# Kernel tuning notes

Hardware: AMD Instinct MI355X
Metric: run time of the kernel (lower is better)

Reference implementation:

```python
import jax, jax.numpy as jnp
import numpy as np


def _rgcn_layer(h, Wr, Ws, src, dst, rel, norm):
    # h: [N,d], Wr: [R,d,d] per-relation weight, Ws: [d,d] self-loop weight
    N, d = h.shape
    R = Wr.shape[0]
    E = src.shape[0]
    msg = jnp.zeros((E, d), h.dtype)
    for r in range(R):  # R is small/static; transform-then-gather per relation
        hW = h @ Wr[r]              # [N,d]
        msg = jnp.where((rel == r)[:, None], hW[src], msg)  # [E,d]
    agg = jax.ops.segment_sum(msg * norm[:, None], dst, num_segments=N)
    return jax.nn.relu(agg + h @ Ws)


def _calc_score(emb, w_relation, es, er, eo):
    # DistMult-style bilinear score: s^T W_r o per target edge
    s = emb[es]                     # [T,d]
    o = emb[eo]                     # [T,d]
    R = w_relation.shape[0]
    sW = jnp.zeros_like(s)
    for r in range(R):
        sW = jnp.where((er == r)[:, None], s @ w_relation[r], sW)
    return jnp.sum(sW * o, axis=-1)  # [T]


def setup_inputs() -> dict:
    key = jax.random.key(0)
    ks = jax.random.split(key, 16)
    N, E, T, d, R, L = 20000, 160000, 50000, 768, 8, 2
    sc = 1.0 / np.sqrt(d)
    return {
        "node_feat": jax.random.normal(ks[0], (N, d), jnp.float32),
        "edge_norm": jax.random.uniform(ks[1], (E,), jnp.float32),
        "W_rel": jax.random.normal(ks[2], (L, R, d, d), jnp.float32) * sc,
        "W_self": jax.random.normal(ks[3], (L, d, d), jnp.float32) * sc,
        "w_relation": jax.random.normal(ks[4], (R, d, d), jnp.float32) * sc,
        "src": jax.random.randint(ks[5], (E,), 0, N, jnp.int32),
        "dst": jax.random.randint(ks[6], (E,), 0, N, jnp.int32),
        "rel": jax.random.randint(ks[7], (E,), 0, R, jnp.int32),
        "pos_src": jax.random.randint(ks[8], (T,), 0, N, jnp.int32),
        "pos_rel": jax.random.randint(ks[9], (T,), 0, R, jnp.int32),
        "pos_dst": jax.random.randint(ks[10], (T,), 0, N, jnp.int32),
        "neg_src": jax.random.randint(ks[11], (T,), 0, N, jnp.int32),
        "neg_rel": jax.random.randint(ks[12], (T,), 0, R, jnp.int32),
        "neg_dst": jax.random.randint(ks[13], (T,), 0, N, jnp.int32),
    }


def reference(node_feat, edge_norm, W_rel, W_self, w_relation,
              src, dst, rel, pos_src, pos_rel, pos_dst,
              neg_src, neg_rel, neg_dst):
    h = node_feat
    L = W_rel.shape[0]
    for l in range(L):
        h = _rgcn_layer(h, W_rel[l], W_self[l], src, dst, rel, edge_norm)
    es = jnp.concatenate([pos_src, neg_src])
    er = jnp.concatenate([pos_rel, neg_rel])
    eo = jnp.concatenate([pos_dst, neg_dst])
    score = _calc_score(h, w_relation, es, er, eo)  # [2T]
    return score
```

## Files before the change

### kernel.cpp

```cpp
#include <hip/hip_runtime.h>

typedef float f32x4 __attribute__((ext_vector_type(4)));
typedef __bf16 bf16x8 __attribute__((ext_vector_type(8)));
typedef unsigned short u16x8 __attribute__((ext_vector_type(8)));
typedef unsigned short u16x4 __attribute__((ext_vector_type(4)));

static __device__ __forceinline__ unsigned short f2bf(float f) {
  unsigned int x = __builtin_bit_cast(unsigned int, f);
  x += 0x7FFFu + ((x >> 16) & 1u);
  return (unsigned short)(x >> 16);
}
static __device__ __forceinline__ float bf2f(unsigned short h) {
  unsigned int x = ((unsigned int)h) << 16;
  return __builtin_bit_cast(float, x);
}

static __device__ __forceinline__ void gload_lds16(const unsigned short* g,
                                                   unsigned short* l) {
  __builtin_amdgcn_global_load_lds(
      (const __attribute__((address_space(1))) void*)g,
      (__attribute__((address_space(3))) void*)l, 16, 0, 0);
}

__global__ __launch_bounds__(256) void k_f32_to_bf16(
    const float* __restrict__ in, unsigned short* __restrict__ out, int n4) {
  int i = blockIdx.x * 256 + threadIdx.x;
  if (i >= n4) return;
  float4 v = reinterpret_cast<const float4*>(in)[i];
  u16x4 o = {f2bf(v.x), f2bf(v.y), f2bf(v.z), f2bf(v.w)};
  reinterpret_cast<u16x4*>(out)[i] = o;
}

__global__ __launch_bounds__(256) void k_transpose_w(
    const float* __restrict__ in, unsigned short* __restrict__ out, int RG) {
  __shared__ float tile[32][33];
  const int D = 768;
  int z = blockIdx.z;
  int j = z % RG, grp = z / RG;
  const float* A = in + (size_t)z * D * D;
  const size_t ld = (size_t)RG * D;
  unsigned short* O = out + (size_t)grp * D * ld + (size_t)j * D;
  int nt = blockIdx.x * 32, kt = blockIdx.y * 32;
  int tx = threadIdx.x, ty = threadIdx.y;
#pragma unroll
  for (int i = 0; i < 4; ++i)
    tile[ty + i * 8][tx] = A[(size_t)(kt + ty + i * 8) * D + nt + tx];
  __syncthreads();
#pragma unroll
  for (int i = 0; i < 4; ++i)
    O[(size_t)(nt + ty + i * 8) * ld + kt + tx] = f2bf(tile[tx][ty + i * 8]);
}

__global__ __launch_bounds__(256) void k_hist(const int* __restrict__ dst,
                                              const int* __restrict__ rel,
                                              int* __restrict__ cnt, int E, int NV) {
  int e = blockIdx.x * 256 + threadIdx.x;
  if (e < E) atomicAdd(&cnt[rel[e] * NV + dst[e]], 1);
}

__global__ __launch_bounds__(256) void k_part(const int* __restrict__ cnt,
                                              int* __restrict__ bsum, int n) {
  __shared__ int wsums[4];
  int blk = blockIdx.x, tid = threadIdx.x;
  int base = blk * 1024 + tid * 4;
  int s = 0;
#pragma unroll
  for (int j = 0; j < 4; ++j) {
    int i = base + j;
    if (i < n) s += cnt[i];
  }
#pragma unroll
  for (int d = 1; d < 64; d <<= 1) s += __shfl_xor(s, d, 64);
  if ((tid & 63) == 0) wsums[tid >> 6] = s;
  __syncthreads();
  if (tid == 0) bsum[blk] = wsums[0] + wsums[1] + wsums[2] + wsums[3];
}

__global__ __launch_bounds__(1024) void k_scan_b(const int* __restrict__ bsum,
                                                 int* __restrict__ bscan, int nb,
                                                 int* __restrict__ off_total) {
  __shared__ int wpre[16];
  int tid = threadIdx.x, lane = tid & 63, w = tid >> 6;
  int v = (tid < nb) ? bsum[tid] : 0;
  int inc = v;
#pragma unroll
  for (int d = 1; d < 64; d <<= 1) {
    int t = __shfl_up(inc, d, 64);
    if (lane >= d) inc += t;
  }
  if (lane == 63) wpre[w] = inc;
  __syncthreads();
  if (w == 0) {
    int vv = (lane < 16) ? wpre[lane] : 0;
    int p = vv;
#pragma unroll
    for (int d = 1; d < 16; d <<= 1) {
      int t = __shfl_up(p, d, 64);
      if (lane >= d) p += t;
    }
    if (lane < 16) wpre[lane] = p - vv;
  }
  __syncthreads();
  if (tid < nb) bscan[tid] = wpre[w] + inc - v;
  if (tid == 1023) *off_total = wpre[15] + inc;
}

__global__ __launch_bounds__(256) void k_scan_f(const int* __restrict__ cnt,
                                                const int* __restrict__ bscan,
                                                int* __restrict__ off, int n) {
  __shared__ int wpre[4];
  int blk = blockIdx.x, tid = threadIdx.x, lane = tid & 63, w = tid >> 6;
  int base = blk * 1024 + tid * 4;
  int v[4];
  int s = 0;
#pragma unroll
  for (int j = 0; j < 4; ++j) {
    int i = base + j;
    v[j] = (i < n) ? cnt[i] : 0;
    s += v[j];
  }
  int inc = s;
#pragma unroll
  for (int d = 1; d < 64; d <<= 1) {
    int t = __shfl_up(inc, d, 64);
    if (lane >= d) inc += t;
  }
  if (lane == 63) wpre[w] = inc;
  __syncthreads();
  int wb = 0;
  for (int j = 0; j < w; ++j) wb += wpre[j];
  int run = bscan[blk] + wb + (inc - s);
#pragma unroll
  for (int j = 0; j < 4; ++j) {
    int i = base + j;
    if (i < n) off[i] = run;
    run += v[j];
  }
}

__global__ __launch_bounds__(256) void k_bucket(
    const int* __restrict__ src, const int* __restrict__ dst,
    const int* __restrict__ rel, const float* __restrict__ norm,
    const int* __restrict__ off, int* __restrict__ fill,
    int* __restrict__ spack, float* __restrict__ snorm, int E, int NV) {
  int e = blockIdx.x * 256 + threadIdx.x;
  if (e >= E) return;
  int key = rel[e] * NV + dst[e];
  int slot = off[key] + atomicAdd(&fill[key], 1);
  spack[slot] = src[e];
  snorm[slot] = norm[e];
}

__global__ __launch_bounds__(256) void k_gather(
    const unsigned short* __restrict__ h, const int* __restrict__ off,
    const int* __restrict__ spack, const float* __restrict__ snorm,
    unsigned short* __restrict__ Acat, int NV, int r0, int r1, int ld) {
  int v = (blockIdx.x * 256 + threadIdx.x) >> 6;
  int lane = threadIdx.x & 63;
  int col = lane * 4;
  for (int r = r0; r < r1; ++r) {
    float a[12];
#pragma unroll
    for (int j = 0; j < 12; ++j) a[j] = 0.f;
    if (v < NV) {
      int beg = off[r * NV + v], end = off[r * NV + v + 1];
      for (int p = beg; p < end; ++p) {
        const unsigned short* row = h + (size_t)spack[p] * 768 + col;
        float nm = snorm[p];
#pragma unroll
        for (int c = 0; c < 3; ++c) {
          u16x4 vv = *reinterpret_cast<const u16x4*>(row + c * 256);
#pragma unroll
          for (int j = 0; j < 4; ++j) a[c * 4 + j] += nm * bf2f(vv[j]);
        }
      }
    }
    unsigned short* orow = Acat + (size_t)v * ld + (size_t)(r - r0) * 768 + col;
#pragma unroll
    for (int c = 0; c < 3; ++c) {
      u16x4 o = {f2bf(a[c * 4 + 0]), f2bf(a[c * 4 + 1]),
                 f2bf(a[c * 4 + 2]), f2bf(a[c * 4 + 3])};
      *reinterpret_cast<u16x4*>(orow + c * 256) = o;
    }
  }
}

#define STAGE_A(BUF, HALF, TT)                                                   \
  do {                                                                           \
    const unsigned short* _s =                                                   \
        A + (size_t)(m0 + (HALF) * 128 + srow) * K + (size_t)(TT) * 64 + gcol;   \
    gload_lds16(_s, &As[BUF][HALF][w << 3][0]);                                  \
    gload_lds16(_s + (size_t)64 * K, &As[BUF][HALF][64 + (w << 3)][0]);          \
  } while (0)
#define STAGE_B(BUF, HALF, TT)                                                   \
  do {                                                                           \
    const unsigned short* _s =                                                   \
        B + (size_t)(n0 + (HALF) * 128 + srow) * K + (size_t)(TT) * 64 + gcol;   \
    gload_lds16(_s, &Bs[BUF][HALF][w << 3][0]);                                  \
    gload_lds16(_s + (size_t)64 * K, &Bs[BUF][HALF][64 + (w << 3)][0]);          \
  } while (0)
#define PHASE(MA, NB, ...)                                                       \
  do {                                                                           \
    bf16x8 af[4][2], bv[2][2];                                                   \
    _Pragma("unroll") for (int i = 0; i < 4; ++i)                                \
        _Pragma("unroll") for (int kk = 0; kk < 2; ++kk)                         \
            af[i][kk] = *reinterpret_cast<const bf16x8*>(                        \
                &As[buf][MA][wr * 64 + i * 16 + lr]                              \
                   [((lg + 4 * kk) ^ (lr & 7)) * 8]);                            \
    _Pragma("unroll") for (int j = 0; j < 2; ++j)                                \
        _Pragma("unroll") for (int kk = 0; kk < 2; ++kk)                         \
            bv[j][kk] = *reinterpret_cast<const bf16x8*>(                        \
                &Bs[buf][NB][wc * 32 + j * 16 + lr]                              \
                   [((lg + 4 * kk) ^ (lr & 7)) * 8]);                            \
    __VA_ARGS__;                                                                 \
    asm volatile("" ::: "memory");                                               \
    __builtin_amdgcn_s_barrier();                                                \
    asm volatile("" ::: "memory");                                               \
    __builtin_amdgcn_s_setprio(1);                                               \
    _Pragma("unroll") for (int i = 0; i < 4; ++i)                                \
        _Pragma("unroll") for (int j = 0; j < 2; ++j)                            \
            _Pragma("unroll") for (int kk = 0; kk < 2; ++kk)                     \
                acc[MA][NB][i][j] = __builtin_amdgcn_mfma_f32_16x16x32_bf16(     \
                    af[i][kk], bv[j][kk], acc[MA][NB][i][j], 0, 0, 0);           \
    __builtin_amdgcn_s_setprio(0);                                               \
    asm volatile("" ::: "memory");                                               \
    __builtin_amdgcn_s_barrier();                                                \
    asm volatile("" ::: "memory");                                               \
  } while (0)

template <int EPI>
__global__ __launch_bounds__(512, 2) void k_gemm_tn(
    const unsigned short* __restrict__ A, const unsigned short* __restrict__ B,
    void* __restrict__ Cp, const float* __restrict__ C0,
    int M, int N, int K, int MT, int NT) {
  __shared__ unsigned short As[2][2][128][64];
  __shared__ unsigned short Bs[2][2][128][64];
  const int tid = threadIdx.x;
  const int lane = tid & 63;
  const int w = tid >> 6;
  const int wr = w >> 2;
  const int wc = w & 3;
  const int lr = lane & 15, lg = lane >> 4;

  int bid = blockIdx.x;
  const int per = 8 * NT;
  int grp = bid / per, rem = bid % per;
  int mstart = grp * 8;
  int gsz = MT - mstart; if (gsz > 8) gsz = 8;
  const int mt = mstart + rem % gsz;
  const int ntile = rem / gsz;
  const int m0 = mt * 256, n0 = ntile * 256;

  const int srow = tid >> 3;
  const int gcol = (((tid & 7) ^ (tid >> 3)) & 7) * 8;

  f32x4 acc[2][2][4][2] = {};
  const int nk = K >> 6;

  STAGE_A(0, 0, 0);
  STAGE_B(0, 1, 0);
  STAGE_A(0, 1, 0);
  STAGE_B(0, 0, 0);
  if (nk > 1) {
    STAGE_A(1, 0, 1);
    STAGE_B(1, 1, 1);
  }

  for (int t = 0; t < nk; ++t) {
    const int buf = t & 1;
    if (t + 1 < nk)
      asm volatile("s_waitcnt vmcnt(4)" ::: "memory");
    else
      asm volatile("s_waitcnt vmcnt(0)" ::: "memory");
    __builtin_amdgcn_s_barrier();
    asm volatile("" ::: "memory");
    PHASE(0, 1, if (t + 1 < nk) STAGE_A(buf ^ 1, 1, t + 1));
    PHASE(0, 0, if (t + 1 < nk) STAGE_B(buf ^ 1, 0, t + 1));
    PHASE(1, 1, if (t + 2 < nk) STAGE_A(buf, 0, t + 2));
    PHASE(1, 0, if (t + 2 < nk) STAGE_B(buf, 1, t + 2));
  }

#pragma unroll
  for (int ma = 0; ma < 2; ++ma)
#pragma unroll
    for (int i = 0; i < 4; ++i)
#pragma unroll
      for (int q = 0; q < 4; ++q) {
        int r = m0 + ma * 128 + wr * 64 + i * 16 + lg * 4 + q;
        if (r >= M) continue;
#pragma unroll
        for (int nb = 0; nb < 2; ++nb)
#pragma unroll
          for (int j = 0; j < 2; ++j) {
            int cn = n0 + nb * 128 + wc * 32 + j * 16 + lr;
            float v = acc[ma][nb][i][j][q];
            size_t idx = (size_t)r * N + cn;
            if (EPI == 0) {
              ((unsigned short*)Cp)[idx] = f2bf(v);
            } else if (EPI == 1) {
              v += C0[idx];
              v = v > 0.f ? v : 0.f;
              ((unsigned short*)Cp)[idx] = f2bf(v);
            } else if (EPI == 2) {
              ((float*)Cp)[idx] = v;
            } else {
              ((float*)Cp)[idx] = v + C0[idx];
            }
          }
      }
}

__global__ __launch_bounds__(256) void k_score(
    const unsigned short* __restrict__ SW, const unsigned short* __restrict__ emb,
    const int* __restrict__ ps, const int* __restrict__ pr, const int* __restrict__ pd,
    const int* __restrict__ ns, const int* __restrict__ nr, const int* __restrict__ nd,
    float* __restrict__ out, int T, int r0, int r1, int ldSW) {
  int t = (blockIdx.x * 256 + threadIdx.x) >> 6;
  if (t >= 2 * T) return;
  int s, r, o;
  if (t < T) { s = ps[t]; r = pr[t]; o = pd[t]; }
  else       { s = ns[t - T]; r = nr[t - T]; o = nd[t - T]; }
  if (r < r0 || r >= r1) return;
  int lane = threadIdx.x & 63;
  int col = lane * 4;
  const unsigned short* a = SW + (size_t)s * ldSW + (size_t)(r - r0) * 768 + col;
  const unsigned short* b = emb + (size_t)o * 768 + col;
  float acc = 0.f;
#pragma unroll
  for (int c = 0; c < 3; ++c) {
    u16x4 va = *reinterpret_cast<const u16x4*>(a + c * 256);
    u16x4 vb = *reinterpret_cast<const u16x4*>(b + c * 256);
#pragma unroll
    for (int j = 0; j < 4; ++j) acc += bf2f(va[j]) * bf2f(vb[j]);
  }
#pragma unroll
  for (int off = 32; off > 0; off >>= 1) acc += __shfl_down(acc, off, 64);
  if (lane == 0) out[t] = acc;
}

extern "C" void kernel_launch(void* const* d_in, const int* in_sizes, int n_in,
                              void* d_out, int out_size, void* d_ws, size_t ws_size,
                              hipStream_t stream) {
  const float* node_feat = (const float*)d_in[0];
  const float* edge_norm = (const float*)d_in[1];
  const float* W_rel = (const float*)d_in[2];
  const float* W_self = (const float*)d_in[3];
  const float* w_relation = (const float*)d_in[4];
  const int* src = (const int*)d_in[5];
  const int* dst = (const int*)d_in[6];
  const int* rel = (const int*)d_in[7];
  const int* pos_src = (const int*)d_in[8];
  const int* pos_rel = (const int*)d_in[9];
  const int* pos_dst = (const int*)d_in[10];
  const int* neg_src = (const int*)d_in[11];
  const int* neg_rel = (const int*)d_in[12];
  const int* neg_dst = (const int*)d_in[13];

  const int D = 768;
  const int NV = in_sizes[0] / D;
  const int E = in_sizes[1];
  const int L = in_sizes[3] / (D * D);
  const int R = in_sizes[4] / (D * D);
  const int T = in_sizes[8];
  const int Mpad = (NV + 255) & ~255;
  const int RN = R * NV;
  const int NB = (RN + 1023) / 1024;

  auto align_up = [](size_t x) { return (x + 255) & ~(size_t)255; };
  size_t sz_wt_rel = align_up((size_t)L * R * D * D * 2);
  size_t sz_wt_self = align_up((size_t)L * D * D * 2);
  size_t sz_wt_score = align_up((size_t)R * D * D * 2);
  size_t sz_h = align_up((size_t)Mpad * D * 2);
  size_t sz_agg = align_up((size_t)Mpad * D * 4);
  size_t sz_cntfill = align_up((size_t)2 * RN * 4);
  size_t sz_off = align_up((size_t)(RN + 8) * 4);
  size_t sz_sp = align_up((size_t)E * 4);
  size_t sz_bs = align_up((size_t)2 * (NB + 8) * 4);
  size_t fixed = sz_wt_rel + sz_wt_self + sz_wt_score + sz_h + sz_agg +
                 sz_cntfill + sz_off + 2 * sz_sp + sz_bs;
  int RG = 4;
  while (RG > 1 && fixed + align_up((size_t)Mpad * RG * D * 2) > ws_size) RG >>= 1;
  const int NGRP = R / RG;

  char* wp = (char*)d_ws;
  unsigned short* wt_rel = (unsigned short*)wp; wp += sz_wt_rel;
  unsigned short* wt_self = (unsigned short*)wp; wp += sz_wt_self;
  unsigned short* wt_score = (unsigned short*)wp; wp += sz_wt_score;
  unsigned short* h = (unsigned short*)wp; wp += sz_h;
  float* agg = (float*)wp; wp += sz_agg;
  int* cnt = (int*)wp; int* fill = cnt + RN; wp += sz_cntfill;
  int* off = (int*)wp; wp += sz_off;
  int* spack = (int*)wp; wp += sz_sp;
  float* snorm = (float*)wp; wp += sz_sp;
  int* bsum = (int*)wp; int* bscan = bsum + NB + 4; wp += sz_bs;
  unsigned short* Acat = (unsigned short*)wp;

  dim3 tb32(32, 8);
  k_f32_to_bf16<<<(NV * D / 4 + 255) / 256, 256, 0, stream>>>(node_feat, h, NV * D / 4);
  if (Mpad > NV)
    hipMemsetAsync(h + (size_t)NV * D, 0, (size_t)(Mpad - NV) * D * 2, stream);
  k_transpose_w<<<dim3(24, 24, L * R), tb32, 0, stream>>>(W_rel, wt_rel, RG);
  k_transpose_w<<<dim3(24, 24, L), tb32, 0, stream>>>(W_self, wt_self, 1);
  k_transpose_w<<<dim3(24, 24, R), tb32, 0, stream>>>(w_relation, wt_score, 1);

  hipMemsetAsync(cnt, 0, (size_t)2 * RN * 4, stream);
  k_hist<<<(E + 255) / 256, 256, 0, stream>>>(dst, rel, cnt, E, NV);
  k_part<<<NB, 256, 0, stream>>>(cnt, bsum, RN);
  k_scan_b<<<1, 1024, 0, stream>>>(bsum, bscan, NB, off + RN);
  k_scan_f<<<NB, 256, 0, stream>>>(cnt, bscan, off, RN);
  k_bucket<<<(E + 255) / 256, 256, 0, stream>>>(src, dst, rel, edge_norm, off, fill,
                                                spack, snorm, E, NV);

  const int MT = Mpad / 256;
  const int KG = RG * D;
  const int gblocks = Mpad / 4;
  for (int l = 0; l < L; ++l) {
    k_gemm_tn<2><<<MT * 3, 512, 0, stream>>>(
        h, wt_self + (size_t)l * D * D, agg, nullptr, NV, D, D, MT, 3);
    for (int gi = 0; gi < NGRP; ++gi) {
      k_gather<<<gblocks, 256, 0, stream>>>(h, off, spack, snorm, Acat, NV,
                                            gi * RG, gi * RG + RG, KG);
      const unsigned short* Bw = wt_rel + (size_t)(l * NGRP + gi) * D * KG;
      if (gi == NGRP - 1)
        k_gemm_tn<1><<<MT * 3, 512, 0, stream>>>(Acat, Bw, h, agg, NV, D, KG, MT, 3);
      else
        k_gemm_tn<3><<<MT * 3, 512, 0, stream>>>(Acat, Bw, agg, agg, NV, D, KG, MT, 3);
    }
  }
  for (int gi = 0; gi < NGRP; ++gi) {
    k_gemm_tn<0><<<MT * RG * 3, 512, 0, stream>>>(
        h, wt_score + (size_t)gi * RG * D * D, Acat, nullptr, NV, KG, D, MT, RG * 3);
    k_score<<<(2 * T + 3) / 4, 256, 0, stream>>>(Acat, h, pos_src, pos_rel, pos_dst,
                                                 neg_src, neg_rel, neg_dst,
                                                 (float*)d_out, T, gi * RG,
                                                 gi * RG + RG, KG);
  }
}
```

Before: 1.013 ms.

## Merge GEMM k-loop phases into two halves, reusing B fragments

The four barrier-separated MFMA phases per k-step become two phases, one per A half. Both B halves are loaded into registers once per k-step instead of twice, which cuts LDS reads and drops the per-iteration barrier count from nine to three. The global-to-LDS staging order stays the same, so the vmcnt accounting still holds. The cost is more live VGPRs for B fragments under a 512-thread, 2-blocks-per-CU launch bound, which risks spills or lower occupancy, and longer MFMA runs between the remaining barriers.

```diff
diff --git a/kernel.cpp b/kernel.cpp
--- a/kernel.cpp
+++ b/kernel.cpp
@@ -199,34 +199,6 @@
     gload_lds16(_s, &Bs[BUF][HALF][w << 3][0]);                                  \
     gload_lds16(_s + (size_t)64 * K, &Bs[BUF][HALF][64 + (w << 3)][0]);          \
   } while (0)
-#define PHASE(MA, NB, ...)                                                       \
-  do {                                                                           \
-    bf16x8 af[4][2], bv[2][2];                                                   \
-    _Pragma("unroll") for (int i = 0; i < 4; ++i)                                \
-        _Pragma("unroll") for (int kk = 0; kk < 2; ++kk)                         \
-            af[i][kk] = *reinterpret_cast<const bf16x8*>(                        \
-                &As[buf][MA][wr * 64 + i * 16 + lr]                              \
-                   [((lg + 4 * kk) ^ (lr & 7)) * 8]);                            \
-    _Pragma("unroll") for (int j = 0; j < 2; ++j)                                \
-        _Pragma("unroll") for (int kk = 0; kk < 2; ++kk)                         \
-            bv[j][kk] = *reinterpret_cast<const bf16x8*>(                        \
-                &Bs[buf][NB][wc * 32 + j * 16 + lr]                              \
-                   [((lg + 4 * kk) ^ (lr & 7)) * 8]);                            \
-    __VA_ARGS__;                                                                 \
-    asm volatile("" ::: "memory");                                               \
-    __builtin_amdgcn_s_barrier();                                                \
-    asm volatile("" ::: "memory");                                               \
-    __builtin_amdgcn_s_setprio(1);                                               \
-    _Pragma("unroll") for (int i = 0; i < 4; ++i)                                \
-        _Pragma("unroll") for (int j = 0; j < 2; ++j)                            \
-            _Pragma("unroll") for (int kk = 0; kk < 2; ++kk)                     \
-                acc[MA][NB][i][j] = __builtin_amdgcn_mfma_f32_16x16x32_bf16(     \
-                    af[i][kk], bv[j][kk], acc[MA][NB][i][j], 0, 0, 0);           \
-    __builtin_amdgcn_s_setprio(0);                                               \
-    asm volatile("" ::: "memory");                                               \
-    __builtin_amdgcn_s_barrier();                                                \
-    asm volatile("" ::: "memory");                                               \
-  } while (0)
 
 template <int EPI>
 __global__ __launch_bounds__(512, 2) void k_gemm_tn(
@@ -266,6 +238,7 @@
     STAGE_B(1, 1, 1);
   }
 
+  bf16x8 af[4][2], bv[2][2][2];
   for (int t = 0; t < nk; ++t) {
     const int buf = t & 1;
     if (t + 1 < nk)
@@ -274,10 +247,61 @@
       asm volatile("s_waitcnt vmcnt(0)" ::: "memory");
     __builtin_amdgcn_s_barrier();
     asm volatile("" ::: "memory");
-    PHASE(0, 1, if (t + 1 < nk) STAGE_A(buf ^ 1, 1, t + 1));
-    PHASE(0, 0, if (t + 1 < nk) STAGE_B(buf ^ 1, 0, t + 1));
-    PHASE(1, 1, if (t + 2 < nk) STAGE_A(buf, 0, t + 2));
-    PHASE(1, 0, if (t + 2 < nk) STAGE_B(buf, 1, t + 2));
+#pragma unroll
+    for (int i = 0; i < 4; ++i)
+#pragma unroll
+      for (int kk = 0; kk < 2; ++kk)
+        af[i][kk] = *reinterpret_cast<const bf16x8*>(
+            &As[buf][0][wr * 64 + i * 16 + lr][((lg + 4 * kk) ^ (lr & 7)) * 8]);
+#pragma unroll
+    for (int nb = 0; nb < 2; ++nb)
+#pragma unroll
+      for (int j = 0; j < 2; ++j)
+#pragma unroll
+        for (int kk = 0; kk < 2; ++kk)
+          bv[nb][j][kk] = *reinterpret_cast<const bf16x8*>(
+              &Bs[buf][nb][wc * 32 + j * 16 + lr][((lg + 4 * kk) ^ (lr & 7)) * 8]);
+    if (t + 1 < nk) {
+      STAGE_A(buf ^ 1, 1, t + 1);
+      STAGE_B(buf ^ 1, 0, t + 1);
+    }
+    __builtin_amdgcn_s_setprio(1);
+#pragma unroll
+    for (int i = 0; i < 4; ++i)
+#pragma unroll
+      for (int nb = 0; nb < 2; ++nb)
+#pragma unroll
+        for (int j = 0; j < 2; ++j)
+#pragma unroll
+          for (int kk = 0; kk < 2; ++kk)
+            acc[0][nb][i][j] = __builtin_amdgcn_mfma_f32_16x16x32_bf16(
+                af[i][kk], bv[nb][j][kk], acc[0][nb][i][j], 0, 0, 0);
+    __builtin_amdgcn_s_setprio(0);
+    asm volatile("" ::: "memory");
+    __builtin_amdgcn_s_barrier();
+    asm volatile("" ::: "memory");
+#pragma unroll
+    for (int i = 0; i < 4; ++i)
+#pragma unroll
+      for (int kk = 0; kk < 2; ++kk)
+        af[i][kk] = *reinterpret_cast<const bf16x8*>(
+            &As[buf][1][wr * 64 + i * 16 + lr][((lg + 4 * kk) ^ (lr & 7)) * 8]);
+    if (t + 2 < nk) {
+      STAGE_A(buf, 0, t + 2);
+      STAGE_B(buf, 1, t + 2);
+    }
+    __builtin_amdgcn_s_setprio(1);
+#pragma unroll
+    for (int i = 0; i < 4; ++i)
+#pragma unroll
+      for (int nb = 0; nb < 2; ++nb)
+#pragma unroll
+        for (int j = 0; j < 2; ++j)
+#pragma unroll
+          for (int kk = 0; kk < 2; ++kk)
+            acc[1][nb][i][j] = __builtin_amdgcn_mfma_f32_16x16x32_bf16(
+                af[i][kk], bv[nb][j][kk], acc[1][nb][i][j], 0, 0, 0);
+    __builtin_amdgcn_s_setprio(0);
   }
 
 #pragma unroll
```

Result: faster. 883.2 us (-12.8%).

## Restructure GEMM mainloop to keep B fragments in registers and interleave A loads

Applied to the files above, without the earlier changes.

The bf16 TN GEMM main loop is rewritten. It now reads all B fragments for a K tile into registers once and streams A fragments through two register slots, interleaved with the MFMA blocks. Barriers drop from five to two per K tile, and the global-to-LDS staging order changes so A halves and B tiles are prefetched at different lookahead distances. The loop is unrolled by two tiles with no tail handling, so it assumes an even number of K tiles, and it holds more fragment registers at once.

```diff
diff --git a/kernel.cpp b/kernel.cpp
--- a/kernel.cpp
+++ b/kernel.cpp
@@ -199,31 +199,56 @@
     gload_lds16(_s, &Bs[BUF][HALF][w << 3][0]);                                  \
     gload_lds16(_s + (size_t)64 * K, &Bs[BUF][HALF][64 + (w << 3)][0]);          \
   } while (0)
-#define PHASE(MA, NB, ...)                                                       \
+#define R_BV(BUF)                                                                \
+  _Pragma("unroll") for (int nb = 0; nb < 2; ++nb)                               \
+  _Pragma("unroll") for (int j = 0; j < 2; ++j)                                  \
+  _Pragma("unroll") for (int kk = 0; kk < 2; ++kk)                               \
+      bv[nb][j][kk] = *reinterpret_cast<const bf16x8*>(                          \
+          &Bs[BUF][nb][wc * 32 + j * 16 + lr][((lg + 4 * kk) ^ (lr & 7)) * 8]);
+#define R_AFRAG(SLOT, BUF, HALF, I)                                              \
+  _Pragma("unroll") for (int kk = 0; kk < 2; ++kk)                               \
+      afs[SLOT][kk] = *reinterpret_cast<const bf16x8*>(                          \
+          &As[BUF][HALF][wr * 64 + (I) * 16 + lr][((lg + 4 * kk) ^ (lr & 7)) * 8]);
+#define MBLOCK(MA, SLOT, I)                                                      \
+  _Pragma("unroll") for (int nb = 0; nb < 2; ++nb)                               \
+  _Pragma("unroll") for (int j = 0; j < 2; ++j)                                  \
+  _Pragma("unroll") for (int kk = 0; kk < 2; ++kk)                               \
+      acc[MA][nb][I][j] = __builtin_amdgcn_mfma_f32_16x16x32_bf16(               \
+          afs[SLOT][kk], bv[nb][j][kk], acc[MA][nb][I][j], 0, 0, 0);
+#define MPHASE(MA, BUF, HALF)                                                    \
   do {                                                                           \
-    bf16x8 af[4][2], bv[2][2];                                                   \
-    _Pragma("unroll") for (int i = 0; i < 4; ++i)                                \
-        _Pragma("unroll") for (int kk = 0; kk < 2; ++kk)                         \
-            af[i][kk] = *reinterpret_cast<const bf16x8*>(                        \
-                &As[buf][MA][wr * 64 + i * 16 + lr]                              \
-                   [((lg + 4 * kk) ^ (lr & 7)) * 8]);                            \
-    _Pragma("unroll") for (int j = 0; j < 2; ++j)                                \
-        _Pragma("unroll") for (int kk = 0; kk < 2; ++kk)                         \
-            bv[j][kk] = *reinterpret_cast<const bf16x8*>(                        \
-                &Bs[buf][NB][wc * 32 + j * 16 + lr]                              \
-                   [((lg + 4 * kk) ^ (lr & 7)) * 8]);                            \
-    __VA_ARGS__;                                                                 \
-    asm volatile("" ::: "memory");                                               \
+    R_AFRAG(0, BUF, HALF, 0);                                                    \
+    __builtin_amdgcn_s_setprio(1);                                               \
+    R_AFRAG(1, BUF, HALF, 1);                                                    \
+    MBLOCK(MA, 0, 0);                                                            \
+    R_AFRAG(0, BUF, HALF, 2);                                                    \
+    MBLOCK(MA, 1, 1);                                                            \
+    R_AFRAG(1, BUF, HALF, 3);                                                    \
+    MBLOCK(MA, 0, 2);                                                            \
+    MBLOCK(MA, 1, 3);                                                            \
+    __builtin_amdgcn_s_setprio(0);                                               \
+  } while (0)
+#define TILE(BUF, T)                                                             \
+  do {                                                                           \
+    STAGE_A(BUF, 1, T);                                               \
+    if ((T) + 1 < nk) STAGE_A(BUF ^ 1, 0, (T) + 1);                 \
+    MPHASE(0, BUF, 0);                              \
+    if ((T) + 1 < nk)                                                            \
+      asm volatile("s_waitcnt vmcnt(2)" ::: "memory");                           \
+    else                                                                         \
+      asm volatile("s_waitcnt vmcnt(0)" ::: "memory");                           \
     __builtin_amdgcn_s_barrier();                                                \
     asm volatile("" ::: "memory");                                               \
-    __builtin_amdgcn_s_setprio(1);                                               \
-    _Pragma("unroll") for (int i = 0; i < 4; ++i)                                \
-        _Pragma("unroll") for (int j = 0; j < 2; ++j)                            \
-            _Pragma("unroll") for (int kk = 0; kk < 2; ++kk)                     \
-                acc[MA][NB][i][j] = __builtin_amdgcn_mfma_f32_16x16x32_bf16(     \
-                    af[i][kk], bv[j][kk], acc[MA][NB][i][j], 0, 0, 0);           \
-    __builtin_amdgcn_s_setprio(0);                                               \
-    asm volatile("" ::: "memory");                                               \
+    if ((T) + 2 < nk) {                                                          \
+      STAGE_B(BUF, 0, (T) + 2);                                     \
+      STAGE_B(BUF, 1, (T) + 2);                                     \
+    }                                                                            \
+    MPHASE(1, BUF, 1);                             \
+    if ((T) + 1 < nk) { R_BV(BUF ^ 1); }              \
+    if ((T) + 2 < nk)                                                            \
+      asm volatile("s_waitcnt vmcnt(4)" ::: "memory");                           \
+    else                                                                         \
+      asm volatile("s_waitcnt vmcnt(0)" ::: "memory");                           \
     __builtin_amdgcn_s_barrier();                                                \
     asm volatile("" ::: "memory");                                               \
   } while (0)
@@ -255,29 +280,27 @@
   const int gcol = (((tid & 7) ^ (tid >> 3)) & 7) * 8;
 
   f32x4 acc[2][2][4][2] = {};
+  bf16x8 bv[2][2][2];
+  bf16x8 afs[2][2];
   const int nk = K >> 6;
 
   STAGE_A(0, 0, 0);
+  STAGE_B(0, 0, 0);
   STAGE_B(0, 1, 0);
-  STAGE_A(0, 1, 0);
-  STAGE_B(0, 0, 0);
   if (nk > 1) {
-    STAGE_A(1, 0, 1);
+    STAGE_B(1, 0, 1);
     STAGE_B(1, 1, 1);
-  }
-
-  for (int t = 0; t < nk; ++t) {
-    const int buf = t & 1;
-    if (t + 1 < nk)
-      asm volatile("s_waitcnt vmcnt(4)" ::: "memory");
-    else
-      asm volatile("s_waitcnt vmcnt(0)" ::: "memory");
-    __builtin_amdgcn_s_barrier();
-    asm volatile("" ::: "memory");
-    PHASE(0, 1, if (t + 1 < nk) STAGE_A(buf ^ 1, 1, t + 1));
-    PHASE(0, 0, if (t + 1 < nk) STAGE_B(buf ^ 1, 0, t + 1));
-    PHASE(1, 1, if (t + 2 < nk) STAGE_A(buf, 0, t + 2));
-    PHASE(1, 0, if (t + 2 < nk) STAGE_B(buf, 1, t + 2));
+    asm volatile("s_waitcnt vmcnt(4)" ::: "memory");
+  } else {
+    asm volatile("s_waitcnt vmcnt(0)" ::: "memory");
+  }
+  __builtin_amdgcn_s_barrier();
+  asm volatile("" ::: "memory");
+  R_BV(0);
+
+  for (int t = 0; t < nk; t += 2) {
+    TILE(0, t);
+    TILE(1, t + 1);
   }
 
 #pragma unroll
```

New measurement: 1.001 ms. No clear change (-1.2%).

## Bucket score targets by relation and fuse gathered GEMM with dot-product epilogue

Applied to the files above, without the earlier changes.

Scoring no longer computes h@W_r for every node and every relation. Target triples are bucketed by relation into 256-row tiles, and a new GEMM gathers the subject rows of h directly into LDS, multiplies them by that tile's relation weight, and fuses the dot product with the object rows into the epilogue using atomic adds into the output. The main GEMM loop is also restructured so each LDS A-fragment is reused across both N halves, which cuts LDS reads and barriers per k-step. This adds histogram, scan and bucketing kernels plus atomics, and tiles padded per relation.

```diff
diff --git a/kernel.cpp b/kernel.cpp
--- a/kernel.cpp
+++ b/kernel.cpp
@@ -183,6 +183,49 @@
       *reinterpret_cast<u16x4*>(orow + c * 256) = o;
     }
   }
+}
+
+__global__ __launch_bounds__(256) void k_thist(
+    const int* __restrict__ pr, const int* __restrict__ nr,
+    int* __restrict__ tcnt, int T) {
+  int t = blockIdx.x * 256 + threadIdx.x;
+  if (t >= 2 * T) return;
+  int r = (t < T) ? pr[t] : nr[t - T];
+  atomicAdd(&tcnt[r], 1);
+}
+
+__global__ void k_tscan(const int* __restrict__ tcnt, int* __restrict__ tpo,
+                        int* __restrict__ btile, int R, int ntiles) {
+  int run = 0;
+  for (int r = 0; r < R; ++r) {
+    tpo[r] = run;
+    run += (tcnt[r] + 255) & ~255;
+  }
+  tpo[R] = run;
+  for (int mt = 0; mt < ntiles; ++mt) {
+    int base = mt * 256;
+    int b = -1;
+    if (base < run)
+      for (int r = 0; r < R; ++r)
+        if (base >= tpo[r] && base < tpo[r + 1]) { b = r; break; }
+    btile[mt] = b;
+  }
+}
+
+__global__ __launch_bounds__(256) void k_tbucket(
+    const int* __restrict__ ps, const int* __restrict__ pr, const int* __restrict__ pd,
+    const int* __restrict__ ns, const int* __restrict__ nr, const int* __restrict__ nd,
+    const int* __restrict__ tpo, int* __restrict__ tfill,
+    int* __restrict__ sidx, int* __restrict__ oidx, int* __restrict__ tmap, int T) {
+  int t = blockIdx.x * 256 + threadIdx.x;
+  if (t >= 2 * T) return;
+  int s, r, o;
+  if (t < T) { s = ps[t]; r = pr[t]; o = pd[t]; }
+  else       { s = ns[t - T]; r = nr[t - T]; o = nd[t - T]; }
+  int slot = tpo[r] + atomicAdd(&tfill[r], 1);
+  sidx[slot] = s;
+  oidx[slot] = o;
+  tmap[slot] = t;
 }
 
 #define STAGE_A(BUF, HALF, TT)                                                   \
@@ -199,34 +242,77 @@
     gload_lds16(_s, &Bs[BUF][HALF][w << 3][0]);                                  \
     gload_lds16(_s + (size_t)64 * K, &Bs[BUF][HALF][64 + (w << 3)][0]);          \
   } while (0)
-#define PHASE(MA, NB, ...)                                                       \
-  do {                                                                           \
-    bf16x8 af[4][2], bv[2][2];                                                   \
-    _Pragma("unroll") for (int i = 0; i < 4; ++i)                                \
-        _Pragma("unroll") for (int kk = 0; kk < 2; ++kk)                         \
-            af[i][kk] = *reinterpret_cast<const bf16x8*>(                        \
-                &As[buf][MA][wr * 64 + i * 16 + lr]                              \
-                   [((lg + 4 * kk) ^ (lr & 7)) * 8]);                            \
-    _Pragma("unroll") for (int j = 0; j < 2; ++j)                                \
-        _Pragma("unroll") for (int kk = 0; kk < 2; ++kk)                         \
-            bv[j][kk] = *reinterpret_cast<const bf16x8*>(                        \
-                &Bs[buf][NB][wc * 32 + j * 16 + lr]                              \
-                   [((lg + 4 * kk) ^ (lr & 7)) * 8]);                            \
-    __VA_ARGS__;                                                                 \
-    asm volatile("" ::: "memory");                                               \
+#define GEMM_PRE()                                                               \
+  const int tid = threadIdx.x;                                                   \
+  const int lane = tid & 63;                                                     \
+  const int w = tid >> 6;                                                        \
+  const int wr = w >> 2;                                                         \
+  const int wc = w & 3;                                                          \
+  const int lr = lane & 15, lg = lane >> 4;                                      \
+  int bid = blockIdx.x;                                                          \
+  const int per = 8 * NT;                                                        \
+  int grp = bid / per, rem = bid % per;                                          \
+  int mstart = grp * 8;                                                          \
+  int gsz = MT - mstart;                                                         \
+  if (gsz > 8) gsz = 8;                                                          \
+  const int mt = mstart + rem % gsz;                                             \
+  const int ntile = rem / gsz;                                                   \
+  const int m0 = mt * 256, n0 = ntile * 256;                                     \
+  const int srow = tid >> 3;                                                     \
+  const int gcol = (((tid & 7) ^ (tid >> 3)) & 7) * 8;                           \
+  const int nk = K >> 6;
+#define R_BV6(BUF)                                                               \
+  _Pragma("unroll") for (int nb = 0; nb < 2; ++nb)                               \
+  _Pragma("unroll") for (int j = 0; j < 2; ++j)                                  \
+  _Pragma("unroll") for (int kk = 0; kk < 2; ++kk)                               \
+      bv[nb][j][kk] = *reinterpret_cast<const bf16x8*>(                          \
+          &Bs[BUF][nb][wc * 32 + j * 16 + lr][((lg + 4 * kk) ^ (lr & 7)) * 8]);
+#define R_AF6(BUF, HALF)                                                         \
+  _Pragma("unroll") for (int i = 0; i < 4; ++i)                                  \
+  _Pragma("unroll") for (int kk = 0; kk < 2; ++kk)                               \
+      af[i][kk] = *reinterpret_cast<const bf16x8*>(                              \
+          &As[BUF][HALF][wr * 64 + i * 16 + lr][((lg + 4 * kk) ^ (lr & 7)) * 8]);
+#define GEMM_LOOP(STAGEA_MACRO)                                                  \
+  bf16x8 af[4][2], bv[2][2][2];                                                  \
+  for (int t = 0; t < nk; ++t) {                                                 \
+    const int buf = t & 1;                                                       \
+    if (t + 1 < nk)                                                              \
+      asm volatile("s_waitcnt vmcnt(4)" ::: "memory");                           \
+    else                                                                         \
+      asm volatile("s_waitcnt vmcnt(0)" ::: "memory");                           \
     __builtin_amdgcn_s_barrier();                                                \
     asm volatile("" ::: "memory");                                               \
+    R_AF6(buf, 0);                                                               \
+    R_BV6(buf);                                                                  \
+    if (t + 1 < nk) {                                                            \
+      STAGEA_MACRO(buf ^ 1, 1, t + 1);                                           \
+      STAGE_B(buf ^ 1, 0, t + 1);                                                \
+    }                                                                            \
     __builtin_amdgcn_s_setprio(1);                                               \
     _Pragma("unroll") for (int i = 0; i < 4; ++i)                                \
-        _Pragma("unroll") for (int j = 0; j < 2; ++j)                            \
-            _Pragma("unroll") for (int kk = 0; kk < 2; ++kk)                     \
-                acc[MA][NB][i][j] = __builtin_amdgcn_mfma_f32_16x16x32_bf16(     \
-                    af[i][kk], bv[j][kk], acc[MA][NB][i][j], 0, 0, 0);           \
+    _Pragma("unroll") for (int nb = 0; nb < 2; ++nb)                             \
+    _Pragma("unroll") for (int j = 0; j < 2; ++j)                                \
+    _Pragma("unroll") for (int kk = 0; kk < 2; ++kk)                             \
+        acc[0][nb][i][j] = __builtin_amdgcn_mfma_f32_16x16x32_bf16(              \
+            af[i][kk], bv[nb][j][kk], acc[0][nb][i][j], 0, 0, 0);                \
     __builtin_amdgcn_s_setprio(0);                                               \
     asm volatile("" ::: "memory");                                               \
     __builtin_amdgcn_s_barrier();                                                \
     asm volatile("" ::: "memory");                                               \
-  } while (0)
+    R_AF6(buf, 1);                                                               \
+    if (t + 2 < nk) {                                                            \
+      STAGEA_MACRO(buf, 0, t + 2);                                               \
+      STAGE_B(buf, 1, t + 2);                                                    \
+    }                                                                            \
+    __builtin_amdgcn_s_setprio(1);                                               \
+    _Pragma("unroll") for (int i = 0; i < 4; ++i)                                \
+    _Pragma("unroll") for (int nb = 0; nb < 2; ++nb)                             \
+    _Pragma("unroll") for (int j = 0; j < 2; ++j)                                \
+    _Pragma("unroll") for (int kk = 0; kk < 2; ++kk)                             \
+        acc[1][nb][i][j] = __builtin_amdgcn_mfma_f32_16x16x32_bf16(              \
+            af[i][kk], bv[nb][j][kk], acc[1][nb][i][j], 0, 0, 0);                \
+    __builtin_amdgcn_s_setprio(0);                                               \
+  }
 
 template <int EPI>
 __global__ __launch_bounds__(512, 2) void k_gemm_tn(
@@ -235,27 +321,8 @@
     int M, int N, int K, int MT, int NT) {
   __shared__ unsigned short As[2][2][128][64];
   __shared__ unsigned short Bs[2][2][128][64];
-  const int tid = threadIdx.x;
-  const int lane = tid & 63;
-  const int w = tid >> 6;
-  const int wr = w >> 2;
-  const int wc = w & 3;
-  const int lr = lane & 15, lg = lane >> 4;
-
-  int bid = blockIdx.x;
-  const int per = 8 * NT;
-  int grp = bid / per, rem = bid % per;
-  int mstart = grp * 8;
-  int gsz = MT - mstart; if (gsz > 8) gsz = 8;
-  const int mt = mstart + rem % gsz;
-  const int ntile = rem / gsz;
-  const int m0 = mt * 256, n0 = ntile * 256;
-
-  const int srow = tid >> 3;
-  const int gcol = (((tid & 7) ^ (tid >> 3)) & 7) * 8;
-
+  GEMM_PRE();
   f32x4 acc[2][2][4][2] = {};
-  const int nk = K >> 6;
 
   STAGE_A(0, 0, 0);
   STAGE_B(0, 1, 0);
@@ -265,20 +332,7 @@
     STAGE_A(1, 0, 1);
     STAGE_B(1, 1, 1);
   }
-
-  for (int t = 0; t < nk; ++t) {
-    const int buf = t & 1;
-    if (t + 1 < nk)
-      asm volatile("s_waitcnt vmcnt(4)" ::: "memory");
-    else
-      asm volatile("s_waitcnt vmcnt(0)" ::: "memory");
-    __builtin_amdgcn_s_barrier();
-    asm volatile("" ::: "memory");
-    PHASE(0, 1, if (t + 1 < nk) STAGE_A(buf ^ 1, 1, t + 1));
-    PHASE(0, 0, if (t + 1 < nk) STAGE_B(buf ^ 1, 0, t + 1));
-    PHASE(1, 1, if (t + 2 < nk) STAGE_A(buf, 0, t + 2));
-    PHASE(1, 0, if (t + 2 < nk) STAGE_B(buf, 1, t + 2));
-  }
+  GEMM_LOOP(STAGE_A);
 
 #pragma unroll
   for (int ma = 0; ma < 2; ++ma)
@@ -310,32 +364,63 @@
       }
 }
 
-__global__ __launch_bounds__(256) void k_score(
-    const unsigned short* __restrict__ SW, const unsigned short* __restrict__ emb,
-    const int* __restrict__ ps, const int* __restrict__ pr, const int* __restrict__ pd,
-    const int* __restrict__ ns, const int* __restrict__ nr, const int* __restrict__ nd,
-    float* __restrict__ out, int T, int r0, int r1, int ldSW) {
-  int t = (blockIdx.x * 256 + threadIdx.x) >> 6;
-  if (t >= 2 * T) return;
-  int s, r, o;
-  if (t < T) { s = ps[t]; r = pr[t]; o = pd[t]; }
-  else       { s = ns[t - T]; r = nr[t - T]; o = nd[t - T]; }
-  if (r < r0 || r >= r1) return;
-  int lane = threadIdx.x & 63;
-  int col = lane * 4;
-  const unsigned short* a = SW + (size_t)s * ldSW + (size_t)(r - r0) * 768 + col;
-  const unsigned short* b = emb + (size_t)o * 768 + col;
-  float acc = 0.f;
-#pragma unroll
-  for (int c = 0; c < 3; ++c) {
-    u16x4 va = *reinterpret_cast<const u16x4*>(a + c * 256);
-    u16x4 vb = *reinterpret_cast<const u16x4*>(b + c * 256);
-#pragma unroll
-    for (int j = 0; j < 4; ++j) acc += bf2f(va[j]) * bf2f(vb[j]);
-  }
-#pragma unroll
-  for (int off = 32; off > 0; off >>= 1) acc += __shfl_down(acc, off, 64);
-  if (lane == 0) out[t] = acc;
+#define STAGE_AI(BUF, HALF, TT)                                                  \
+  do {                                                                           \
+    gload_lds16(pa##HALF##a + (size_t)(TT) * 64, &As[BUF][HALF][w << 3][0]);     \
+    gload_lds16(pa##HALF##b + (size_t)(TT) * 64,                                 \
+                &As[BUF][HALF][64 + (w << 3)][0]);                               \
+  } while (0)
+
+__global__ __launch_bounds__(512, 2) void k_gemm_score(
+    const unsigned short* __restrict__ h, const unsigned short* __restrict__ Bw,
+    float* __restrict__ out, const int* __restrict__ sidx,
+    const int* __restrict__ oidx, const int* __restrict__ tmap,
+    const int* __restrict__ btile, int MT, int NT) {
+  const int K = 768;
+  __shared__ unsigned short As[2][2][128][64];
+  __shared__ unsigned short Bs[2][2][128][64];
+  GEMM_PRE();
+  const int bt = btile[mt];
+  if (bt < 0) return;
+  const unsigned short* B = Bw + (size_t)bt * K * K;
+  const unsigned short* pa0a = h + (size_t)sidx[m0 + srow] * K + gcol;
+  const unsigned short* pa0b = h + (size_t)sidx[m0 + 64 + srow] * K + gcol;
+  const unsigned short* pa1a = h + (size_t)sidx[m0 + 128 + srow] * K + gcol;
+  const unsigned short* pa1b = h + (size_t)sidx[m0 + 192 + srow] * K + gcol;
+
+  f32x4 acc[2][2][4][2] = {};
+
+  STAGE_AI(0, 0, 0);
+  STAGE_B(0, 1, 0);
+  STAGE_AI(0, 1, 0);
+  STAGE_B(0, 0, 0);
+  STAGE_AI(1, 0, 1);
+  STAGE_B(1, 1, 1);
+  GEMM_LOOP(STAGE_AI);
+
+#pragma unroll
+  for (int ma = 0; ma < 2; ++ma)
+#pragma unroll
+    for (int i = 0; i < 4; ++i)
+#pragma unroll
+      for (int q = 0; q < 4; ++q) {
+        int slot = m0 + ma * 128 + wr * 64 + i * 16 + lg * 4 + q;
+        int t = tmap[slot];
+        float p = 0.f;
+        if (t >= 0) {
+          const unsigned short* orow = h + (size_t)oidx[slot] * K;
+#pragma unroll
+          for (int nb = 0; nb < 2; ++nb)
+#pragma unroll
+            for (int j = 0; j < 2; ++j) {
+              int cn = n0 + nb * 128 + wc * 32 + j * 16 + lr;
+              p += acc[ma][nb][i][j][q] * bf2f(orow[cn]);
+            }
+        }
+#pragma unroll
+        for (int d = 1; d < 16; d <<= 1) p += __shfl_xor(p, d, 64);
+        if (t >= 0 && lr == 0) unsafeAtomicAdd(&out[t], p);
+      }
 }
 
 extern "C" void kernel_launch(void* const* d_in, const int* in_sizes, int n_in,
@@ -365,6 +450,8 @@
   const int Mpad = (NV + 255) & ~255;
   const int RN = R * NV;
   const int NB = (RN + 1023) / 1024;
+  const int TB = (2 * T + R * 256 + 255) / 256;
+  const int Mbound = TB * 256;
 
   auto align_up = [](size_t x) { return (x + 255) & ~(size_t)255; };
   size_t sz_wt_rel = align_up((size_t)L * R * D * D * 2);
@@ -376,8 +463,11 @@
   size_t sz_off = align_up((size_t)(RN + 8) * 4);
   size_t sz_sp = align_up((size_t)E * 4);
   size_t sz_bs = align_up((size_t)2 * (NB + 8) * 4);
+  size_t sz_tix = align_up((size_t)Mbound * 4);
+  size_t sz_tsmall = align_up((size_t)(TB + 64) * 4);
   size_t fixed = sz_wt_rel + sz_wt_self + sz_wt_score + sz_h + sz_agg +
-                 sz_cntfill + sz_off + 2 * sz_sp + sz_bs;
+                 sz_cntfill + sz_off + 2 * sz_sp + sz_bs + 3 * sz_tix +
+                 sz_tsmall;
   int RG = 4;
   while (RG > 1 && fixed + align_up((size_t)Mpad * RG * D * 2) > ws_size) RG >>= 1;
   const int NGRP = R / RG;
@@ -393,6 +483,14 @@
   int* spack = (int*)wp; wp += sz_sp;
   float* snorm = (float*)wp; wp += sz_sp;
   int* bsum = (int*)wp; int* bscan = bsum + NB + 4; wp += sz_bs;
+  int* sidx = (int*)wp; wp += sz_tix;
+  int* oidx = (int*)wp; wp += sz_tix;
+  int* tmap = (int*)wp; wp += sz_tix;
+  int* btile = (int*)wp;
+  int* tcnt = btile + TB + 8;
+  int* tfill = tcnt + R + 8;
+  int* tpo = tfill + R + 8;
+  wp += sz_tsmall;
   unsigned short* Acat = (unsigned short*)wp;
 
   dim3 tb32(32, 8);
@@ -410,6 +508,16 @@
   k_scan_f<<<NB, 256, 0, stream>>>(cnt, bscan, off, RN);
   k_bucket<<<(E + 255) / 256, 256, 0, stream>>>(src, dst, rel, edge_norm, off, fill,
                                                 spack, snorm, E, NV);
+
+  hipMemsetAsync(tcnt, 0, (size_t)(2 * R + 8) * 4, stream);
+  hipMemsetAsync(sidx, 0, sz_tix, stream);
+  hipMemsetAsync(tmap, 0xFF, sz_tix, stream);
+  hipMemsetAsync(d_out, 0, (size_t)2 * T * 4, stream);
+  k_thist<<<(2 * T + 255) / 256, 256, 0, stream>>>(pos_rel, neg_rel, tcnt, T);
+  k_tscan<<<1, 1, 0, stream>>>(tcnt, tpo, btile, R, TB);
+  k_tbucket<<<(2 * T + 255) / 256, 256, 0, stream>>>(
+      pos_src, pos_rel, pos_dst, neg_src, neg_rel, neg_dst,
+      tpo, tfill, sidx, oidx, tmap, T);
 
   const int MT = Mpad / 256;
   const int KG = RG * D;
@@ -427,12 +535,6 @@
         k_gemm_tn<3><<<MT * 3, 512, 0, stream>>>(Acat, Bw, agg, agg, NV, D, KG, MT, 3);
     }
   }
-  for (int gi = 0; gi < NGRP; ++gi) {
-    k_gemm_tn<0><<<MT * RG * 3, 512, 0, stream>>>(
-        h, wt_score + (size_t)gi * RG * D * D, Acat, nullptr, NV, KG, D, MT, RG * 3);
-    k_score<<<(2 * T + 3) / 4, 256, 0, stream>>>(Acat, h, pos_src, pos_rel, pos_dst,
-                                                 neg_src, neg_rel, neg_dst,
-                                                 (float*)d_out, T, gi * RG,
-                                                 gi * RG + RG, KG);
-  }
-}
+  k_gemm_score<<<TB * 3, 512, 0, stream>>>(h, wt_score, (float*)d_out,
+                                           sidx, oidx, tmap, btile, TB, 3);
+}
```

After: 2.046 ms. +101.9%, slower.
